# Performance work log

Hardware: AMD Instinct MI355X
Metric: run time of the kernel (lower is better)

The kernel has to match this reference:

```python
import jax, jax.numpy as jnp
import numpy as np

N = 4096        # nodes
IN_DIM = 256    # input feature dim
HID = 64        # hidden per head (num_hidden_layers)
HEADS = 8
OUT_DIM = 64
ALPHA = 0.2     # LeakyReLU negative slope
NEG_INF = jnp.float32(-9e15)


def setup_inputs() -> dict:
    key = jax.random.key(0)
    ks = jax.random.split(key, 8)
    x = jax.random.normal(ks[0], (N, IN_DIM), dtype=jnp.float32)
    adj = (jax.random.uniform(ks[1], (N, N)) < 0.002).astype(jnp.float32)
    adj = jnp.maximum(adj, jnp.eye(N, dtype=jnp.float32))
    s = 0.1
    W_h = jax.random.normal(ks[2], (HEADS, IN_DIM, HID), dtype=jnp.float32) * s
    a1_h = jax.random.normal(ks[3], (HEADS, HID), dtype=jnp.float32) * s
    a2_h = jax.random.normal(ks[4], (HEADS, HID), dtype=jnp.float32) * s
    W_o = jax.random.normal(ks[5], (HEADS * HID, OUT_DIM), dtype=jnp.float32) * s
    a1_o = jax.random.normal(ks[6], (OUT_DIM,), dtype=jnp.float32) * s
    a2_o = jax.random.normal(ks[7], (OUT_DIM,), dtype=jnp.float32) * s
    return dict(x=x, adj=adj, W_h=W_h, a1_h=a1_h, a2_h=a2_h, W_o=W_o, a1_o=a1_o, a2_o=a2_o)


def _gat_heads(x, adj, W, a1, a2):
    """Multi-head GAT layer. x:[N,F], adj:[N,N], W:[H,F,O], a1/a2:[H,O] -> [H,N,O]."""
    Wh = jnp.einsum('nf,hfo->hno', x, W)                      # [H,N,O]
    f1 = jnp.einsum('hno,ho->hn', Wh, a1)                     # source scores
    f2 = jnp.einsum('hno,ho->hn', Wh, a2)                     # target scores
    e = jax.nn.leaky_relu(f1[:, :, None] + f2[:, None, :], ALPHA)  # [H,N,N]
    e = jnp.where(adj[None] > 0, e, NEG_INF)
    attn = jax.nn.softmax(e, axis=-1)                         # segment-softmax over neighbors
    return jnp.einsum('hnm,hmo->hno', attn, Wh)


def reference(x, adj, W_h, a1_h, a2_h, W_o, a1_o, a2_o):
    # dropout p=0.0 -> identity (deterministic reference)
    h = _gat_heads(x, adj, W_h, a1_h, a2_h)                   # [H,N,HID]
    h = jnp.transpose(h, (1, 0, 2)).reshape(N, HEADS * HID)   # concat heads on dim=-1
    out = _gat_heads(h, adj, W_o[None], a1_o[None], a2_o[None])[0]  # [N,OUT_DIM]
    return jax.nn.elu(out)
```

## Files before the change

kernel.cpp:

```cpp
#include <hip/hip_runtime.h>
#include <cstdint>
#include <cstddef>

#define N_NODES 4096
#define IN_DIM 256
#define HID 64
#define HEADS 8
#define OUT_DIM 64
#define ALPHA 0.2f
#define MAXDEG 64
#define TILE 8

typedef __attribute__((ext_vector_type(8))) short bf16x8;
typedef __attribute__((ext_vector_type(4))) float f32x4;

__device__ __forceinline__ unsigned short f2bf(float f) {
    unsigned u = __float_as_uint(f);
    u += 0x7fffu + ((u >> 16) & 1u);
    return (unsigned short)(u >> 16);
}
__device__ __forceinline__ float bf2f(unsigned short u) {
    return __uint_as_float(((unsigned)u) << 16);
}

__global__ __launch_bounds__(256) void k1_gemm_csr(const float* __restrict__ x,
                                                   const float* __restrict__ W,
                                                   const float* __restrict__ a1,
                                                   const float* __restrict__ a2,
                                                   unsigned short* __restrict__ Whb,
                                                   float* __restrict__ f1,
                                                   float* __restrict__ f2,
                                                   const float* __restrict__ adj,
                                                   int* __restrict__ degs,
                                                   int* __restrict__ cols,
                                                   const float* __restrict__ Wo,
                                                   unsigned short* __restrict__ WoT) {
    __shared__ __attribute__((aligned(16))) unsigned short axs[64][72];
    __shared__ __attribute__((aligned(16))) unsigned short bws[64][72];
    int bid = blockIdx.x;
    int t = threadIdx.x;
    int w = t >> 6, l = t & 63;
    if (bid >= 4608) {
        int k0 = (bid - 4608) * 16;
        #pragma unroll
        for (int i = 0; i < 4; ++i) {
            int e = t + i * 256;
            int kk = k0 + (e >> 6);
            int o = e & 63;
            WoT[(size_t)o * 512 + kk] = f2bf(Wo[(size_t)kk * OUT_DIM + o]);
        }
        return;
    }
    if (bid % 9 == 0) {
        int g = bid / 9;
        int h = g & 7;
        int n0 = (g >> 3) * 64;
        int m0 = (w >> 1) * 32;
        int np = (w & 1) * 32;
        f32x4 zf = {0.f, 0.f, 0.f, 0.f};
        f32x4 acc[2][2] = {{zf, zf}, {zf, zf}};
        const float4* x4 = (const float4*)x;
        const float4* w4 = (const float4*)(W + (size_t)h * IN_DIM * HID);
        for (int kc = 0; kc < IN_DIM; kc += 64) {
            __syncthreads();
            #pragma unroll
            for (int i = 0; i < 4; ++i) {
                int e = t + i * 256;
                int r = e >> 4, c4 = e & 15;
                float4 v = x4[(size_t)(n0 + r) * (IN_DIM / 4) + (kc >> 2) + c4];
                ushort4 u;
                u.x = f2bf(v.x); u.y = f2bf(v.y); u.z = f2bf(v.z); u.w = f2bf(v.w);
                *(ushort4*)&axs[r][c4 * 4] = u;
            }
            #pragma unroll
            for (int i = 0; i < 4; ++i) {
                int e = t + i * 256;
                int kk = e >> 4, c4 = e & 15;
                float4 v = w4[(size_t)(kc + kk) * (HID / 4) + c4];
                bws[4 * c4 + 0][kk] = f2bf(v.x);
                bws[4 * c4 + 1][kk] = f2bf(v.y);
                bws[4 * c4 + 2][kk] = f2bf(v.z);
                bws[4 * c4 + 3][kk] = f2bf(v.w);
            }
            __syncthreads();
            #pragma unroll
            for (int k0 = 0; k0 < 64; k0 += 32) {
                bf16x8 af[2], bfr[2];
                #pragma unroll
                for (int m = 0; m < 2; ++m)
                    af[m] = *(const bf16x8*)&axs[m0 + m * 16 + (l & 15)][k0 + (l >> 4) * 8];
                #pragma unroll
                for (int n = 0; n < 2; ++n)
                    bfr[n] = *(const bf16x8*)&bws[np + n * 16 + (l & 15)][k0 + (l >> 4) * 8];
                #pragma unroll
                for (int m = 0; m < 2; ++m)
                    #pragma unroll
                    for (int n = 0; n < 2; ++n)
                        acc[m][n] = __builtin_amdgcn_mfma_f32_16x16x32_bf16(af[m], bfr[n], acc[m][n], 0, 0, 0);
            }
        }
        __syncthreads();
        float a1c[2], a2c[2];
        #pragma unroll
        for (int n = 0; n < 2; ++n) {
            a1c[n] = a1[h * HID + np + n * 16 + (l & 15)];
            a2c[n] = a2[h * HID + np + n * 16 + (l & 15)];
        }
        float* fred = (float*)&axs[0][0];
        int wn = w & 1;
        #pragma unroll
        for (int m = 0; m < 2; ++m) {
            #pragma unroll
            for (int r = 0; r < 4; ++r) {
                int row = m0 + m * 16 + (l >> 4) * 4 + r;
                #pragma unroll
                for (int n = 0; n < 2; ++n)
                    Whb[((size_t)(n0 + row) * HEADS + h) * HID + np + n * 16 + (l & 15)] =
                        f2bf(acc[m][n][r]);
                float s1 = acc[m][0][r] * a1c[0] + acc[m][1][r] * a1c[1];
                float s2 = acc[m][0][r] * a2c[0] + acc[m][1][r] * a2c[1];
                #pragma unroll
                for (int off = 8; off; off >>= 1) {
                    s1 += __shfl_xor(s1, off);
                    s2 += __shfl_xor(s2, off);
                }
                if ((l & 15) == 0) {
                    fred[0 * 128 + wn * 64 + row] = s1;
                    fred[1 * 128 + wn * 64 + row] = s2;
                }
            }
        }
        __syncthreads();
        if (t < 64) {
            f1[(size_t)(n0 + t) * HEADS + h] = fred[t] + fred[64 + t];
            f2[(size_t)(n0 + t) * HEADS + h] = fred[128 + t] + fred[192 + t];
        }
    } else {
        int g = bid / 9, r9 = bid % 9;
        int row = g * 8 + r9 - 1;
        int* wcols = (int*)&axs[0][0];
        int* wcnt  = (int*)&bws[0][0];
        const float4* arow = (const float4*)(adj + (size_t)row * N_NODES);
        float4 v0 = arow[w * 256 + 0 * 64 + l];
        float4 v1 = arow[w * 256 + 1 * 64 + l];
        float4 v2 = arow[w * 256 + 2 * 64 + l];
        float4 v3 = arow[w * 256 + 3 * 64 + l];
        int base = 0;
        float4 vv[4] = {v0, v1, v2, v3};
        #pragma unroll
        for (int i = 0; i < 4; ++i) {
            float comp[4] = {vv[i].x, vv[i].y, vv[i].z, vv[i].w};
            #pragma unroll
            for (int q = 0; q < 4; ++q) {
                bool pred = comp[q] > 0.f;
                unsigned long long mask = __ballot(pred);
                if (pred) {
                    int pos = base + __popcll(mask & ((1ull << l) - 1ull));
                    if (pos < MAXDEG) wcols[w * MAXDEG + pos] = (w * 256 + i * 64 + l) * 4 + q;
                }
                base += __popcll(mask);
            }
        }
        if (l == 0) wcnt[w] = base < MAXDEG ? base : MAXDEG;
        __syncthreads();
        int c0 = wcnt[0], c1 = wcnt[1], c2 = wcnt[2], c3 = wcnt[3];
        int off = (w > 0 ? c0 : 0) + (w > 1 ? c1 : 0) + (w > 2 ? c2 : 0);
        int mycnt = wcnt[w];
        if (l < mycnt) {
            int gpos = off + l;
            if (gpos < MAXDEG) cols[row * MAXDEG + gpos] = wcols[w * MAXDEG + l];
        }
        if (t == 0) {
            int tot = c0 + c1 + c2 + c3;
            degs[row] = tot < MAXDEG ? tot : MAXDEG;
        }
    }
}

__global__ __launch_bounds__(256) void attn1_gemm2(const unsigned short* __restrict__ Whb,
                                                   const float* __restrict__ f1,
                                                   const float* __restrict__ f2,
                                                   const int* __restrict__ degs,
                                                   const int* __restrict__ cols,
                                                   const unsigned short* __restrict__ WoT,
                                                   const float* __restrict__ a1,
                                                   const float* __restrict__ a2,
                                                   float* __restrict__ Wh2,
                                                   float* __restrict__ f1o,
                                                   float* __restrict__ f2o) {
    __shared__ int   cols_s[TILE][MAXDEG];
    __shared__ int   deg_s[TILE];
    __shared__ float p_s[TILE][HEADS][MAXDEG];
    __shared__ __attribute__((aligned(16))) unsigned short htile[16][520];
    __shared__ __attribute__((aligned(16))) unsigned short bws[64][136];
    __shared__ float fred[2][4][TILE];

    int n0 = blockIdx.x * TILE;
    int t = threadIdx.x;
    int w = t >> 6, l = t & 63;

    if (t < TILE) deg_s[t] = degs[n0 + t];
    {
        int nl = t >> 5, ix = t & 31;
        cols_s[nl][ix]      = cols[(size_t)(n0 + nl) * MAXDEG + ix];
        cols_s[nl][ix + 32] = cols[(size_t)(n0 + nl) * MAXDEG + ix + 32];
    }
    {
        uint4 z = {0u, 0u, 0u, 0u};
        #pragma unroll
        for (int i = 0; i < 2; ++i) {
            int e = t + i * 256;
            int r = 8 + (e >> 6), c8 = e & 63;
            *(uint4*)&htile[r][c8 * 8] = z;
        }
    }
    __syncthreads();

    if (t < TILE * HEADS) {
        int nl = t >> 3, h = t & 7;
        int deg = deg_s[nl];
        float f1v = f1[(size_t)(n0 + nl) * HEADS + h];
        float m = -1e30f;
        for (int j = 0; j < deg; ++j) {
            int c = cols_s[nl][j];
            float v = f1v + f2[(size_t)c * HEADS + h];
            v = v > 0.f ? v : ALPHA * v;
            p_s[nl][h][j] = v;
            m = fmaxf(m, v);
        }
        float s = 0.f;
        for (int j = 0; j < deg; ++j) {
            float p = expf(p_s[nl][h][j] - m);
            p_s[nl][h][j] = p;
            s += p;
        }
        float inv = 1.f / s;
        for (int j = 0; j < deg; ++j) p_s[nl][h][j] *= inv;
    }
    __syncthreads();

    {
        int nl = t >> 5, s = t & 31;
        int deg = deg_s[nl];
        int hA = s >> 3, hB = 4 + (s >> 3);
        float accA[8] = {}, accB[8] = {};
        const uint4* whp = (const uint4*)Whb;
        int j = 0;
        for (; j + 2 <= deg; j += 2) {
            int c0 = cols_s[nl][j], c1 = cols_s[nl][j + 1];
            uint4 u0a = whp[(size_t)c0 * 64 + s];
            uint4 u0b = whp[(size_t)c0 * 64 + 32 + s];
            uint4 u1a = whp[(size_t)c1 * 64 + s];
            uint4 u1b = whp[(size_t)c1 * 64 + 32 + s];
            float p0a = p_s[nl][hA][j],     p0b = p_s[nl][hB][j];
            float p1a = p_s[nl][hA][j + 1], p1b = p_s[nl][hB][j + 1];
            const unsigned short* w0a = (const unsigned short*)&u0a;
            const unsigned short* w0b = (const unsigned short*)&u0b;
            const unsigned short* w1a = (const unsigned short*)&u1a;
            const unsigned short* w1b = (const unsigned short*)&u1b;
            #pragma unroll
            for (int q = 0; q < 8; ++q) {
                accA[q] += p0a * bf2f(w0a[q]) + p1a * bf2f(w1a[q]);
                accB[q] += p0b * bf2f(w0b[q]) + p1b * bf2f(w1b[q]);
            }
        }
        if (j < deg) {
            int c0 = cols_s[nl][j];
            uint4 u0a = whp[(size_t)c0 * 64 + s];
            uint4 u0b = whp[(size_t)c0 * 64 + 32 + s];
            float p0a = p_s[nl][hA][j], p0b = p_s[nl][hB][j];
            const unsigned short* w0a = (const unsigned short*)&u0a;
            const unsigned short* w0b = (const unsigned short*)&u0b;
            #pragma unroll
            for (int q = 0; q < 8; ++q) {
                accA[q] += p0a * bf2f(w0a[q]);
                accB[q] += p0b * bf2f(w0b[q]);
            }
        }
        unsigned short ovA[8], ovB[8];
        #pragma unroll
        for (int q = 0; q < 8; ++q) { ovA[q] = f2bf(accA[q]); ovB[q] = f2bf(accB[q]); }
        *(uint4*)&htile[nl][s * 8]       = *(const uint4*)ovA;
        *(uint4*)&htile[nl][256 + s * 8] = *(const uint4*)ovB;
    }

    f32x4 gacc = {0.f, 0.f, 0.f, 0.f};
    int nbase = w * 16;
    for (int kc = 0; kc < HEADS * HID; kc += 128) {
        __syncthreads();
        #pragma unroll
        for (int i = 0; i < 4; ++i) {
            int e = t + i * 256;
            int o = e >> 4, c8 = e & 15;
            *(uint4*)&bws[o][c8 * 8] = *(const uint4*)&WoT[(size_t)o * 512 + kc + c8 * 8];
        }
        __syncthreads();
        #pragma unroll
        for (int k0 = 0; k0 < 128; k0 += 32) {
            bf16x8 af = *(const bf16x8*)&htile[l & 15][kc + k0 + (l >> 4) * 8];
            bf16x8 bfr = *(const bf16x8*)&bws[nbase + (l & 15)][k0 + (l >> 4) * 8];
            gacc = __builtin_amdgcn_mfma_f32_16x16x32_bf16(af, bfr, gacc, 0, 0, 0);
        }
    }
    float a1c = a1[nbase + (l & 15)];
    float a2c = a2[nbase + (l & 15)];
    #pragma unroll
    for (int r = 0; r < 4; ++r) {
        int row = (l >> 4) * 4 + r;
        float s1 = gacc[r] * a1c;
        float s2 = gacc[r] * a2c;
        #pragma unroll
        for (int off = 8; off; off >>= 1) {
            s1 += __shfl_xor(s1, off);
            s2 += __shfl_xor(s2, off);
        }
        if (row < TILE) {
            Wh2[(size_t)(n0 + row) * OUT_DIM + nbase + (l & 15)] = gacc[r];
            if ((l & 15) == 0) {
                fred[0][w][row] = s1;
                fred[1][w][row] = s2;
            }
        }
    }
    __syncthreads();
    if (t < TILE) {
        f1o[n0 + t] = fred[0][0][t] + fred[0][1][t] + fred[0][2][t] + fred[0][3][t];
        f2o[n0 + t] = fred[1][0][t] + fred[1][1][t] + fred[1][2][t] + fred[1][3][t];
    }
}

__global__ __launch_bounds__(256) void attn2(const float* __restrict__ Wh,
                                             const float* __restrict__ f1,
                                             const float* __restrict__ f2,
                                             const int* __restrict__ degs,
                                             const int* __restrict__ cols,
                                             float* __restrict__ out) {
    int wave = threadIdx.x >> 6;
    int lane = threadIdx.x & 63;
    int n = blockIdx.x * 4 + wave;
    if (n >= N_NODES) return;
    int deg = degs[n];
    int col = 0;
    float e = -1e30f;
    if (lane < deg) {
        col = cols[n * MAXDEG + lane];
        float v = f1[n] + f2[col];
        e = v > 0.f ? v : ALPHA * v;
    }
    float m = e;
    #pragma unroll
    for (int off = 32; off; off >>= 1) m = fmaxf(m, __shfl_xor(m, off));
    float p = (lane < deg) ? expf(e - m) : 0.f;
    float s = p;
    #pragma unroll
    for (int off = 32; off; off >>= 1) s += __shfl_xor(s, off);
    float inv = 1.f / s;
    float acc = 0.f;
    int j = 0;
    for (; j + 8 <= deg; j += 8) {
        int cj[8]; float pj[8]; float v[8];
        #pragma unroll
        for (int q = 0; q < 8; ++q) cj[q] = __shfl(col, j + q);
        #pragma unroll
        for (int q = 0; q < 8; ++q) pj[q] = __shfl(p, j + q);
        #pragma unroll
        for (int q = 0; q < 8; ++q) v[q] = Wh[(size_t)cj[q] * OUT_DIM + lane];
        #pragma unroll
        for (int q = 0; q < 8; ++q) acc += pj[q] * v[q];
    }
    for (; j < deg; ++j) {
        int cj = __shfl(col, j);
        float pj = __shfl(p, j);
        acc += pj * Wh[(size_t)cj * OUT_DIM + lane];
    }
    acc *= inv;
    acc = acc > 0.f ? acc : expf(acc) - 1.f;
    out[(size_t)n * OUT_DIM + lane] = acc;
}

extern "C" void kernel_launch(void* const* d_in, const int* in_sizes, int n_in,
                              void* d_out, int out_size, void* d_ws, size_t ws_size,
                              hipStream_t stream) {
    const float* x    = (const float*)d_in[0];
    const float* adj  = (const float*)d_in[1];
    const float* W_h  = (const float*)d_in[2];
    const float* a1_h = (const float*)d_in[3];
    const float* a2_h = (const float*)d_in[4];
    const float* W_o  = (const float*)d_in[5];
    const float* a1_o = (const float*)d_in[6];
    const float* a2_o = (const float*)d_in[7];
    float* out = (float*)d_out;

    float* wsf  = (float*)d_ws;
    float* Wh2  = wsf;
    float* f1_1 = Wh2 + (size_t)N_NODES * OUT_DIM;
    float* f2_1 = f1_1 + (size_t)N_NODES * HEADS;
    float* f1_2 = f2_1 + (size_t)N_NODES * HEADS;
    float* f2_2 = f1_2 + N_NODES;
    int*   degs = (int*)(f2_2 + N_NODES);
    int*   csr  = degs + N_NODES;
    unsigned short* Whb = (unsigned short*)(csr + (size_t)N_NODES * MAXDEG);
    unsigned short* WoT = Whb + (size_t)N_NODES * HEADS * HID;

    k1_gemm_csr<<<4640, 256, 0, stream>>>(x, W_h, a1_h, a2_h, Whb, f1_1, f2_1,
                                          adj, degs, csr, W_o, WoT);

    attn1_gemm2<<<N_NODES / TILE, 256, 0, stream>>>(Whb, f1_1, f2_1, degs, csr,
                                                    WoT, a1_o, a2_o, Wh2, f1_2, f2_2);

    attn2<<<N_NODES / 4, 256, 0, stream>>>(Wh2, f1_2, f2_2, degs, csr, out);
}
```

Before: 48.85 us.

## Fuse attention-1/GEMM2 with attention-2 via grid barrier, store Wh2 as bf16

Merges the second and third kernels into one persistent launch of 512 blocks, joined by an atomic grid-wide barrier, so one kernel launch and its tail are removed. It also gathers the neighbour f2 scores into shared memory with all threads before the per-head softmax, using a padded [node][j][head] layout. The intermediate Wh2 is stored in bf16 to halve the gather traffic in the second attention. The grid barrier relies on all 512 blocks being co-resident and adds a memset, and bf16 Wh2 reduces precision.

```diff
diff --git a/kernel.cpp b/kernel.cpp
--- a/kernel.cpp
+++ b/kernel.cpp
@@ -10,6 +10,7 @@
 #define ALPHA 0.2f
 #define MAXDEG 64
 #define TILE 8
+#define GRID2 512
 
 typedef __attribute__((ext_vector_type(8))) short bf16x8;
 typedef __attribute__((ext_vector_type(4))) float f32x4;
@@ -177,20 +178,37 @@
     }
 }
 
-__global__ __launch_bounds__(256) void attn1_gemm2(const unsigned short* __restrict__ Whb,
-                                                   const float* __restrict__ f1,
-                                                   const float* __restrict__ f2,
-                                                   const int* __restrict__ degs,
-                                                   const int* __restrict__ cols,
-                                                   const unsigned short* __restrict__ WoT,
-                                                   const float* __restrict__ a1,
-                                                   const float* __restrict__ a2,
-                                                   float* __restrict__ Wh2,
-                                                   float* __restrict__ f1o,
-                                                   float* __restrict__ f2o) {
+__device__ __forceinline__ void grid_barrier(int* bar) {
+    __syncthreads();
+    if (threadIdx.x == 0) {
+        __threadfence();
+        if (atomicAdd(bar + 1, 1) == GRID2 - 1) {
+            atomicExch(bar, 1);
+        } else {
+            while (atomicAdd(bar, 0) < 1) __builtin_amdgcn_s_sleep(1);
+        }
+        __threadfence();
+    }
+    __syncthreads();
+}
+
+__global__ __launch_bounds__(256) void attn1_gemm2_attn2(const unsigned short* __restrict__ Whb,
+                                                         const float* __restrict__ f1,
+                                                         const float* __restrict__ f2,
+                                                         const int* __restrict__ degs,
+                                                         const int* __restrict__ cols,
+                                                         const unsigned short* __restrict__ WoT,
+                                                         const float* __restrict__ a1,
+                                                         const float* __restrict__ a2,
+                                                         unsigned short* __restrict__ Wh2b,
+                                                         float* __restrict__ f1o,
+                                                         float* __restrict__ f2o,
+                                                         float* __restrict__ out,
+                                                         int* __restrict__ bar) {
     __shared__ int   cols_s[TILE][MAXDEG];
     __shared__ int   deg_s[TILE];
-    __shared__ float p_s[TILE][HEADS][MAXDEG];
+    __shared__ float f1s[TILE * HEADS];
+    __shared__ float pf[TILE][65][8];
     __shared__ __attribute__((aligned(16))) unsigned short htile[16][520];
     __shared__ __attribute__((aligned(16))) unsigned short bws[64][136];
     __shared__ float fred[2][4][TILE];
@@ -200,6 +218,7 @@
     int w = t >> 6, l = t & 63;
 
     if (t < TILE) deg_s[t] = degs[n0 + t];
+    if (t < TILE * HEADS) f1s[t] = f1[(size_t)n0 * HEADS + t];
     {
         int nl = t >> 5, ix = t & 31;
         cols_s[nl][ix]      = cols[(size_t)(n0 + nl) * MAXDEG + ix];
@@ -216,26 +235,38 @@
     }
     __syncthreads();
 
+    #pragma unroll
+    for (int it = 0; it < 16; ++it) {
+        int slot = t + it * 256;
+        int nl = slot >> 9;
+        int rem = slot & 511;
+        int j = rem >> 3, h = rem & 7;
+        if (j < deg_s[nl]) {
+            int c = cols_s[nl][j];
+            pf[nl][j][h] = f2[(size_t)c * HEADS + h];
+        }
+    }
+    __syncthreads();
+
     if (t < TILE * HEADS) {
         int nl = t >> 3, h = t & 7;
         int deg = deg_s[nl];
-        float f1v = f1[(size_t)(n0 + nl) * HEADS + h];
+        float f1v = f1s[t];
         float m = -1e30f;
         for (int j = 0; j < deg; ++j) {
-            int c = cols_s[nl][j];
-            float v = f1v + f2[(size_t)c * HEADS + h];
+            float v = f1v + pf[nl][j][h];
             v = v > 0.f ? v : ALPHA * v;
-            p_s[nl][h][j] = v;
+            pf[nl][j][h] = v;
             m = fmaxf(m, v);
         }
         float s = 0.f;
         for (int j = 0; j < deg; ++j) {
-            float p = expf(p_s[nl][h][j] - m);
-            p_s[nl][h][j] = p;
+            float p = expf(pf[nl][j][h] - m);
+            pf[nl][j][h] = p;
             s += p;
         }
         float inv = 1.f / s;
-        for (int j = 0; j < deg; ++j) p_s[nl][h][j] *= inv;
+        for (int j = 0; j < deg; ++j) pf[nl][j][h] *= inv;
     }
     __syncthreads();
 
@@ -252,8 +283,8 @@
             uint4 u0b = whp[(size_t)c0 * 64 + 32 + s];
             uint4 u1a = whp[(size_t)c1 * 64 + s];
             uint4 u1b = whp[(size_t)c1 * 64 + 32 + s];
-            float p0a = p_s[nl][hA][j],     p0b = p_s[nl][hB][j];
-            float p1a = p_s[nl][hA][j + 1], p1b = p_s[nl][hB][j + 1];
+            float p0a = pf[nl][j][hA],     p0b = pf[nl][j][hB];
+            float p1a = pf[nl][j + 1][hA], p1b = pf[nl][j + 1][hB];
             const unsigned short* w0a = (const unsigned short*)&u0a;
             const unsigned short* w0b = (const unsigned short*)&u0b;
             const unsigned short* w1a = (const unsigned short*)&u1a;
@@ -268,7 +299,7 @@
             int c0 = cols_s[nl][j];
             uint4 u0a = whp[(size_t)c0 * 64 + s];
             uint4 u0b = whp[(size_t)c0 * 64 + 32 + s];
-            float p0a = p_s[nl][hA][j], p0b = p_s[nl][hB][j];
+            float p0a = pf[nl][j][hA], p0b = pf[nl][j][hB];
             const unsigned short* w0a = (const unsigned short*)&u0a;
             const unsigned short* w0b = (const unsigned short*)&u0b;
             #pragma unroll
@@ -315,7 +346,7 @@
             s2 += __shfl_xor(s2, off);
         }
         if (row < TILE) {
-            Wh2[(size_t)(n0 + row) * OUT_DIM + nbase + (l & 15)] = gacc[r];
+            Wh2b[(size_t)(n0 + row) * OUT_DIM + nbase + (l & 15)] = f2bf(gacc[r]);
             if ((l & 15) == 0) {
                 fred[0][w][row] = s1;
                 fred[1][w][row] = s2;
@@ -327,55 +358,50 @@
         f1o[n0 + t] = fred[0][0][t] + fred[0][1][t] + fred[0][2][t] + fred[0][3][t];
         f2o[n0 + t] = fred[1][0][t] + fred[1][1][t] + fred[1][2][t] + fred[1][3][t];
     }
-}
-
-__global__ __launch_bounds__(256) void attn2(const float* __restrict__ Wh,
-                                             const float* __restrict__ f1,
-                                             const float* __restrict__ f2,
-                                             const int* __restrict__ degs,
-                                             const int* __restrict__ cols,
-                                             float* __restrict__ out) {
-    int wave = threadIdx.x >> 6;
-    int lane = threadIdx.x & 63;
-    int n = blockIdx.x * 4 + wave;
-    if (n >= N_NODES) return;
-    int deg = degs[n];
-    int col = 0;
-    float e = -1e30f;
-    if (lane < deg) {
-        col = cols[n * MAXDEG + lane];
-        float v = f1[n] + f2[col];
-        e = v > 0.f ? v : ALPHA * v;
-    }
-    float m = e;
+
+    grid_barrier(bar);
+
     #pragma unroll
-    for (int off = 32; off; off >>= 1) m = fmaxf(m, __shfl_xor(m, off));
-    float p = (lane < deg) ? expf(e - m) : 0.f;
-    float s = p;
-    #pragma unroll
-    for (int off = 32; off; off >>= 1) s += __shfl_xor(s, off);
-    float inv = 1.f / s;
-    float acc = 0.f;
-    int j = 0;
-    for (; j + 8 <= deg; j += 8) {
-        int cj[8]; float pj[8]; float v[8];
-        #pragma unroll
-        for (int q = 0; q < 8; ++q) cj[q] = __shfl(col, j + q);
-        #pragma unroll
-        for (int q = 0; q < 8; ++q) pj[q] = __shfl(p, j + q);
-        #pragma unroll
-        for (int q = 0; q < 8; ++q) v[q] = Wh[(size_t)cj[q] * OUT_DIM + lane];
-        #pragma unroll
-        for (int q = 0; q < 8; ++q) acc += pj[q] * v[q];
-    }
-    for (; j < deg; ++j) {
-        int cj = __shfl(col, j);
-        float pj = __shfl(p, j);
-        acc += pj * Wh[(size_t)cj * OUT_DIM + lane];
-    }
-    acc *= inv;
-    acc = acc > 0.f ? acc : expf(acc) - 1.f;
-    out[(size_t)n * OUT_DIM + lane] = acc;
+    for (int rep = 0; rep < 2; ++rep) {
+        int n = blockIdx.x * 8 + rep * 4 + w;
+        int deg = degs[n];
+        int col = 0;
+        float e = -1e30f;
+        if (l < deg) {
+            col = cols[(size_t)n * MAXDEG + l];
+            float v = f1o[n] + f2o[col];
+            e = v > 0.f ? v : ALPHA * v;
+        }
+        float m = e;
+        #pragma unroll
+        for (int off = 32; off; off >>= 1) m = fmaxf(m, __shfl_xor(m, off));
+        float p = (l < deg) ? expf(e - m) : 0.f;
+        float s = p;
+        #pragma unroll
+        for (int off = 32; off; off >>= 1) s += __shfl_xor(s, off);
+        float inv = 1.f / s;
+        float acc = 0.f;
+        int j = 0;
+        for (; j + 8 <= deg; j += 8) {
+            int cj[8]; float pj[8]; float v[8];
+            #pragma unroll
+            for (int q = 0; q < 8; ++q) cj[q] = __shfl(col, j + q);
+            #pragma unroll
+            for (int q = 0; q < 8; ++q) pj[q] = __shfl(p, j + q);
+            #pragma unroll
+            for (int q = 0; q < 8; ++q) v[q] = bf2f(Wh2b[(size_t)cj[q] * OUT_DIM + l]);
+            #pragma unroll
+            for (int q = 0; q < 8; ++q) acc += pj[q] * v[q];
+        }
+        for (; j < deg; ++j) {
+            int cj = __shfl(col, j);
+            float pj = __shfl(p, j);
+            acc += pj * bf2f(Wh2b[(size_t)cj * OUT_DIM + l]);
+        }
+        acc *= inv;
+        acc = acc > 0.f ? acc : expf(acc) - 1.f;
+        out[(size_t)n * OUT_DIM + l] = acc;
+    }
 }
 
 extern "C" void kernel_launch(void* const* d_in, const int* in_sizes, int n_in,
@@ -391,22 +417,24 @@
     const float* a2_o = (const float*)d_in[7];
     float* out = (float*)d_out;
 
-    float* wsf  = (float*)d_ws;
-    float* Wh2  = wsf;
-    float* f1_1 = Wh2 + (size_t)N_NODES * OUT_DIM;
+    int*   bar  = (int*)d_ws;
+    float* wsf  = (float*)((char*)d_ws + 64);
+    float* f1_1 = wsf;
     float* f2_1 = f1_1 + (size_t)N_NODES * HEADS;
     float* f1_2 = f2_1 + (size_t)N_NODES * HEADS;
     float* f2_2 = f1_2 + N_NODES;
     int*   degs = (int*)(f2_2 + N_NODES);
     int*   csr  = degs + N_NODES;
-    unsigned short* Whb = (unsigned short*)(csr + (size_t)N_NODES * MAXDEG);
-    unsigned short* WoT = Whb + (size_t)N_NODES * HEADS * HID;
+    unsigned short* Whb  = (unsigned short*)(csr + (size_t)N_NODES * MAXDEG);
+    unsigned short* WoT  = Whb + (size_t)N_NODES * HEADS * HID;
+    unsigned short* Wh2b = WoT + (size_t)OUT_DIM * HEADS * HID;
+
+    hipMemsetAsync(d_ws, 0, 64, stream);
 
     k1_gemm_csr<<<4640, 256, 0, stream>>>(x, W_h, a1_h, a2_h, Whb, f1_1, f2_1,
                                           adj, degs, csr, W_o, WoT);
 
-    attn1_gemm2<<<N_NODES / TILE, 256, 0, stream>>>(Whb, f1_1, f2_1, degs, csr,
-                                                    WoT, a1_o, a2_o, Wh2, f1_2, f2_2);
-
-    attn2<<<N_NODES / 4, 256, 0, stream>>>(Wh2, f1_2, f2_2, degs, csr, out);
-}
+    attn1_gemm2_attn2<<<GRID2, 256, 0, stream>>>(Whb, f1_1, f2_1, degs, csr,
+                                                 WoT, a1_o, a2_o, Wh2b, f1_2, f2_2,
+                                                 out, bar);
+}
```

New measurement: 93.80 us. +92.0%, slower.
